# Kernel tuning notes

Hardware: AMD Instinct MI355X
Metric: run time of the kernel (lower is better)

Reference implementation:

```python
import jax, jax.numpy as jnp
import numpy as np
from jax import lax

N, C, F, W = 4096, 1, 15, 120
STRIDE = 10
NW = W // STRIDE            # 12 windows
P = F * (F - 1) // 2        # 105 pairs
HP = 2 * P + 4 * F          # 270 stacked stat rows
FC1_IN = 16 * HP * (NW - 2) # 43200
FC2, FC3, FCAST = 512, 128, 1
BN_EPS = 1e-5

# static pair indices, same order as generate(list(range(F)))
_II, _JJ = np.triu_indices(F, k=1)


def _fill(x):
    # numpy_fill: replace nan/inf with 0
    return jnp.where(jnp.isfinite(x), x, jnp.zeros_like(x))


def setup_inputs() -> dict:
    key = jax.random.key(0)
    ks = jax.random.split(key, 13)
    inp = {
        'data': jax.random.uniform(ks[0], (N, C, F, W), dtype=jnp.float32),
        'bn_gamma': jax.random.normal(ks[1], (C,), dtype=jnp.float32),
        'bn_beta': jax.random.normal(ks[2], (C,), dtype=jnp.float32),
        'bn_mean': jax.random.normal(ks[3], (C,), dtype=jnp.float32) * 0.1,
        'bn_var': jax.random.uniform(ks[4], (C,), dtype=jnp.float32) + 0.5,
        'conv_w': jax.random.normal(ks[5], (16, 1, 1, 3), dtype=jnp.float32) * 0.1,
        'conv_b': jax.random.normal(ks[6], (16,), dtype=jnp.float32) * 0.1,
        'fc1_w': jax.random.normal(ks[7], (FC2, FC1_IN), dtype=jnp.float32) * (1.0 / np.sqrt(FC1_IN)),
        'fc1_b': jax.random.normal(ks[8], (FC2,), dtype=jnp.float32) * 0.01,
        'fc2_w': jax.random.normal(ks[9], (FC3, FC2), dtype=jnp.float32) * (1.0 / np.sqrt(FC2)),
        'fc2_b': jax.random.normal(ks[10], (FC3,), dtype=jnp.float32) * 0.01,
        'fc3_w': jax.random.normal(ks[11], (FCAST, FC3), dtype=jnp.float32) * (1.0 / np.sqrt(FC3)),
        'fc3_b': jax.random.normal(ks[12], (FCAST,), dtype=jnp.float32) * 0.01,
    }
    return inp


def _features(data):
    # data: [N,C,F,W] -> windows [N,C,F,NW,S]
    S = STRIDE
    win = data.reshape(data.shape[0], data.shape[1], F, NW, S)
    mean = win.mean(axis=-1)                         # [N,C,F,NW]
    spread = win - mean[..., None]
    var_u = (spread * spread).sum(axis=-1) / (S - 1)  # unbiased, matches torch .std()
    std = jnp.sqrt(var_u)
    # pairwise cov / corr over (II, JJ)
    cov = (spread[:, :, _II] * spread[:, :, _JJ]).sum(axis=-1) / (S - 1)  # [N,C,P,NW]
    corr = _fill(cov / (std[:, :, _II] * std[:, :, _JJ]) * ((S - 1) / S))
    cov = _fill(cov)
    stdf = _fill(std)
    zs = _fill(mean / std)
    ret = _fill(win[..., -1] / win[..., 0] - 1.0)
    w = jnp.arange(1, S + 1, dtype=jnp.float32)
    w = w / w.sum()
    dl = _fill((win * w).sum(axis=-1))
    # concat along feature rows, order as in forward: corr,cov,std,zscore,return,decaylinear
    return jnp.concatenate([corr, cov, stdf, zs, ret, dl], axis=2)  # [N,C,HP,NW]


def reference(data, bn_gamma, bn_beta, bn_mean, bn_var, conv_w, conv_b,
              fc1_w, fc1_b, fc2_w, fc2_b, fc3_w, fc3_b):
    feat = _features(data)  # [N,1,HP,NW]
    # BatchNorm2d (eval mode, running stats)
    x = (feat - bn_mean[None, :, None, None]) * lax.rsqrt(bn_var + BN_EPS)[None, :, None, None]
    x = x * bn_gamma[None, :, None, None] + bn_beta[None, :, None, None]
    # Conv2d(1,16,(1,3)) valid padding
    x = lax.conv_general_dilated(x, conv_w, window_strides=(1, 1), padding='VALID',
                                 dimension_numbers=('NCHW', 'OIHW', 'NCHW'))
    x = jax.nn.relu(x + conv_b[None, :, None, None])  # [N,16,HP,NW-2]
    x = x.reshape(x.shape[0], -1)                      # [N, FC1_IN]
    # MLP head (dropout = identity in eval)
    x = jax.nn.relu(x @ fc1_w.T + fc1_b)
    x = jax.nn.sigmoid(x @ fc2_w.T + fc2_b)
    out = (x @ fc3_w.T + fc3_b)[:, 0]                  # fc3(...).T[0] -> [N]
    return out
```

## Files before the change

### kernel.cpp

```cpp
#include <hip/hip_runtime.h>
#include <cstdint>
#include <cstddef>


typedef _Float16 f16;
typedef f16 f16x2 __attribute__((ext_vector_type(2)));
typedef f16 f16x8 __attribute__((ext_vector_type(8)));
typedef float f32x4 __attribute__((ext_vector_type(4)));

#define CHUNK   2048
#define K_FC1   43200
#define KT_TOT  675
#define TILE_F  16384
#define HALF_F  8192

__device__ __forceinline__ float fillv(float x) { return isfinite(x) ? x : 0.0f; }

__global__ __launch_bounds__(256) void retile_w(const float* __restrict__ w,
                                                f16* __restrict__ Wt) {
    const int bid = blockIdx.x;
    const int nt = bid / KT_TOT, kt = bid % KT_TOT;
    const int t = threadIdx.x;
    f16* dst = Wt + (size_t)bid * TILE_F;
    #pragma unroll
    for (int j = 0; j < 8; ++j) {
        int q = t + 256 * j;
        int half = q >> 10, rr = (q >> 3) & 127, c = q & 7;
        const float* s = w + (size_t)(nt * 256 + half * 128 + rr) * K_FC1 + kt * 64 + c * 8;
        float4 x = *(const float4*)s;
        float4 y = *(const float4*)(s + 4);
        f16x8 o = { (f16)x.x, (f16)x.y, (f16)x.z, (f16)x.w,
                    (f16)y.x, (f16)y.y, (f16)y.z, (f16)y.w };
        int p = c ^ (rr & 7);
        *(f16x8*)(dst + (size_t)half * HALF_F + rr * 64 + p * 8) = o;
    }
}

__global__ __launch_bounds__(256) void stage_a(
    const float* __restrict__ data, const float* __restrict__ bn_g,
    const float* __restrict__ bn_b, const float* __restrict__ bn_m,
    const float* __restrict__ bn_v, const float* __restrict__ conv_w,
    const float* __restrict__ conv_b, f16* __restrict__ A16, int n0)
{
    __shared__ __align__(16) float pool[5400];
    __shared__ __align__(16) float feat[270 * 12];
    __shared__ float cwf[48];
    __shared__ float cbf[16];
    __shared__ int   pi[105], pj[105];

    float* raw = pool;
    f16*   cstage = (f16*)pool;

    const int t = threadIdx.x;
    const int n = n0 + blockIdx.x;
    const float4* src4 = (const float4*)(data + (size_t)n * 1800);
    for (int i = t; i < 450; i += 256) ((float4*)pool)[i] = src4[i];

    {
        float a  = bn_g[0] * rsqrtf(bn_v[0] + 1e-5f);
        float bb = bn_b[0] - bn_m[0] * a;
        if (t < 48) cwf[t] = conv_w[t] * a;
        if (t < 16) cbf[t] = conv_b[t] + bb * (conv_w[3 * t] + conv_w[3 * t + 1] + conv_w[3 * t + 2]);
    }
    if (t < 105) {
        int i = 0, rem = t;
        while (rem >= 14 - i) { rem -= 14 - i; ++i; }
        pi[t] = i; pj[t] = i + 1 + rem;
    }
    __syncthreads();

    if (t < 180) {
        int f = t / 12, w = t % 12;
        int base = f * 120 + w * 10;
        const float2* r2 = (const float2*)(raw + base);
        float2 p0 = r2[0], p1 = r2[1], p2 = r2[2], p3 = r2[3], p4 = r2[4];
        float x[10] = { p0.x, p0.y, p1.x, p1.y, p2.x, p2.y, p3.x, p3.y, p4.x, p4.y };
        float sum = 0.f;
        #pragma unroll
        for (int s = 0; s < 10; ++s) sum += x[s];
        float mean = sum * 0.1f;
        float ret = x[9] / x[0] - 1.0f;
        float dl = 0.f;
        #pragma unroll
        for (int s = 0; s < 10; ++s) dl += x[s] * ((float)(s + 1) * (1.0f / 55.0f));
        float var = 0.f;
        float d[10];
        #pragma unroll
        for (int s = 0; s < 10; ++s) { d[s] = x[s] - mean; var += d[s] * d[s]; }
        float2* w2p = (float2*)(raw + base);
        #pragma unroll
        for (int s = 0; s < 5; ++s) w2p[s] = make_float2(d[2 * s], d[2 * s + 1]);
        var *= (1.0f / 9.0f);
        float sd = sqrtf(var);
        feat[(210 + f) * 12 + w] = fillv(sd);
        feat[(225 + f) * 12 + w] = fillv(mean / sd);
        feat[(240 + f) * 12 + w] = fillv(ret);
        feat[(255 + f) * 12 + w] = fillv(dl);
    }
    __syncthreads();

    for (int q = t; q < 1260; q += 256) {
        int p = q / 12, w = q % 12;
        int i = pi[p], j = pj[p];
        const float2* ri = (const float2*)(raw + i * 120 + w * 10);
        const float2* rj = (const float2*)(raw + j * 120 + w * 10);
        float cv = 0.f;
        #pragma unroll
        for (int s = 0; s < 5; ++s) {
            float2 ai = ri[s], aj = rj[s];
            cv += ai.x * aj.x + ai.y * aj.y;
        }
        cv *= (1.0f / 9.0f);
        float si = feat[(210 + i) * 12 + w], sj = feat[(210 + j) * 12 + w];
        feat[p * 12 + w]         = fillv(cv / (si * sj) * 0.9f);
        feat[(105 + p) * 12 + w] = fillv(cv);
    }
    __syncthreads();

    const int s_idx = blockIdx.x;
    const int mt = s_idx >> 8, r256 = s_idx & 255;
    const int half = r256 >> 7, rloc = r256 & 127, rsw = r256 & 7;
    f16* abase = A16 + ((size_t)(mt * KT_TOT) * 2 + half) * HALF_F + (size_t)rloc * 64;

    for (int p = 0; p < 4; ++p) {
        #pragma unroll
        for (int j = 0; j < 5; ++j) {
            int item = t + (j << 8);
            if (item < 1080) {
                int h = item >> 2, ocl = item & 3, oc = (p << 2) + ocl;
                const float4* f4 = (const float4*)(feat + h * 12);
                float4 fa = f4[0], fb = f4[1], fc = f4[2];
                float fv[12] = { fa.x, fa.y, fa.z, fa.w,
                                 fb.x, fb.y, fb.z, fb.w,
                                 fc.x, fc.y, fc.z, fc.w };
                float w0 = cwf[oc * 3], w1 = cwf[oc * 3 + 1], w2 = cwf[oc * 3 + 2];
                float bz = cbf[oc];
                int kl = ocl * 2700 + h * 10;
                #pragma unroll
                for (int q = 0; q < 5; ++q) {
                    float y0 = fmaf(w2, fv[2 * q + 2], fmaf(w1, fv[2 * q + 1], fmaf(w0, fv[2 * q], bz)));
                    float y1 = fmaf(w2, fv[2 * q + 3], fmaf(w1, fv[2 * q + 2], fmaf(w0, fv[2 * q + 1], bz)));
                    y0 = fminf(fmaxf(y0, 0.f) * 0.00390625f, 65000.f);
                    y1 = fminf(fmaxf(y1, 0.f) * 0.00390625f, 65000.f);
                    *(f16x2*)(cstage + kl + 2 * q) = f16x2{ (f16)y0, (f16)y1 };
                }
            }
        }
        __syncthreads();
        #pragma unroll
        for (int j = 0; j < 6; ++j) {
            int u = t + (j << 8);
            if (u < 1350) {
                int U = p * 1350 + u;
                int kt = U >> 3, c = U & 7;
                f16x8 ov = *(const f16x8*)(cstage + u * 8);
                *(f16x8*)(abase + (size_t)kt * TILE_F + ((c ^ rsw) << 3)) = ov;
            }
        }
        __syncthreads();
    }
}

__global__ __launch_bounds__(512, 2) void gemm_fc1(const f16* __restrict__ A,
                                                   const f16* __restrict__ W,
                                                   float* __restrict__ Ysum)
{
    extern __shared__ f16 lds[];

    const int bid = blockIdx.x;
    const int mt = bid & 7;
    const int slot = bid >> 3;
    const int nt = slot & 1;
    const int sk = slot >> 1;
    const int kt0 = sk * 42 + (sk < 3 ? sk : 3);
    const int cnt = 42 + (sk < 3 ? 1 : 0);

    const int tid = threadIdx.x;
    const int wave = tid >> 6, lane = tid & 63;
    const int quad = lane >> 4, m16 = lane & 15;
    const int rsw = m16 & 7;
    const int wm = (wave & 1) << 6;
    const int wn = (wave >> 1) << 5;

    const f16* Ab = A + (size_t)(mt * KT_TOT + kt0) * TILE_F;
    const f16* Bb = W + (size_t)(nt * KT_TOT + kt0) * TILE_F;

    f32x4 acc[8][4] = {};
    f16x8 a[4][2], bA[2][2], bB[2][2];

#define STAGE_A(BUF, HALF, KI) do {                                            \
    const f16* g_ = Ab + (size_t)(KI) * TILE_F + (HALF) * HALF_F + tid * 8;    \
    f16* l_ = lds + (BUF) * TILE_F + (HALF) * HALF_F + tid * 8;                \
    __builtin_amdgcn_global_load_lds(                                          \
        (const __attribute__((address_space(1))) void*)g_,                     \
        (__attribute__((address_space(3))) void*)l_, 16, 0, 0);                \
    __builtin_amdgcn_global_load_lds(                                          \
        (const __attribute__((address_space(1))) void*)(g_ + 4096),            \
        (__attribute__((address_space(3))) void*)(l_ + 4096), 16, 0, 0);       \
} while (0)

#define STAGE_B(BUF, HALF, KI) do {                                            \
    const f16* g_ = Bb + (size_t)(KI) * TILE_F + (HALF) * HALF_F + tid * 8;    \
    f16* l_ = lds + 32768 + (BUF) * TILE_F + (HALF) * HALF_F + tid * 8;        \
    __builtin_amdgcn_global_load_lds(                                          \
        (const __attribute__((address_space(1))) void*)g_,                     \
        (__attribute__((address_space(3))) void*)l_, 16, 0, 0);                \
    __builtin_amdgcn_global_load_lds(                                          \
        (const __attribute__((address_space(1))) void*)(g_ + 4096),            \
        (__attribute__((address_space(3))) void*)(l_ + 4096), 16, 0, 0);       \
} while (0)

#define RD_A(MH, BUF) do {                                                     \
    _Pragma("unroll") for (int i2_ = 0; i2_ < 4; ++i2_)                        \
    _Pragma("unroll") for (int kh_ = 0; kh_ < 2; ++kh_)                        \
        a[i2_][kh_] = *(const f16x8*)(lds + (BUF) * TILE_F + (MH) * HALF_F     \
            + (wm + i2_ * 16 + m16) * 64 + (((kh_ * 4 + quad) ^ rsw) << 3));   \
} while (0)

#define RD_B(DST, NH, BUF) do {                                                \
    _Pragma("unroll") for (int j2_ = 0; j2_ < 2; ++j2_)                        \
    _Pragma("unroll") for (int kh_ = 0; kh_ < 2; ++kh_)                        \
        DST[j2_][kh_] = *(const f16x8*)(lds + 32768 + (BUF) * TILE_F           \
            + (NH) * HALF_F                                                    \
            + (wn + j2_ * 16 + m16) * 64 + (((kh_ * 4 + quad) ^ rsw) << 3));   \
} while (0)

#define MMA(IO, JO, BF) do {                                                   \
    _Pragma("unroll") for (int i2_ = 0; i2_ < 4; ++i2_)                        \
    _Pragma("unroll") for (int j2_ = 0; j2_ < 2; ++j2_)                        \
    _Pragma("unroll") for (int kh_ = 0; kh_ < 2; ++kh_)                        \
        acc[(IO) + i2_][(JO) + j2_] = __builtin_amdgcn_mfma_f32_16x16x32_f16(  \
            a[i2_][kh_], BF[j2_][kh_], acc[(IO) + i2_][(JO) + j2_], 0, 0, 0);  \
} while (0)

    STAGE_A(0, 0, 0);
    STAGE_B(0, 0, 0);
    STAGE_B(0, 1, 0);
    STAGE_A(0, 1, 0);
    asm volatile("s_waitcnt vmcnt(0)" ::: "memory");
    __builtin_amdgcn_s_barrier();

    #pragma unroll 1
    for (int ti = 0; ti < cnt; ++ti) {
        const int bc = ti & 1, bn = bc ^ 1;
        if (ti + 1 < cnt) {
            STAGE_A(bn, 0, ti + 1);
            STAGE_B(bn, 0, ti + 1);
            STAGE_B(bn, 1, ti + 1);
            STAGE_A(bn, 1, ti + 1);
        }
        RD_A(0, bc); RD_B(bA, 0, bc);
        __builtin_amdgcn_s_setprio(1);
        MMA(0, 0, bA);
        __builtin_amdgcn_s_setprio(0);
        RD_B(bB, 1, bc);
        __builtin_amdgcn_s_setprio(1);
        MMA(0, 2, bB);
        __builtin_amdgcn_s_setprio(0);
        RD_A(1, bc);
        __builtin_amdgcn_s_setprio(1);
        MMA(4, 2, bB);
        MMA(4, 0, bA);
        __builtin_amdgcn_s_setprio(0);
        if (ti + 1 < cnt) {
            asm volatile("s_waitcnt vmcnt(0)" ::: "memory");
            __builtin_amdgcn_s_barrier();
        }
    }

#undef STAGE_A
#undef STAGE_B
#undef RD_A
#undef RD_B
#undef MMA

    float* Yb = Ysum + (size_t)(mt * 256) * 512 + nt * 256;
    #pragma unroll
    for (int i = 0; i < 8; ++i) {
        const int row0 = (i >> 2) * 128 + wm + (i & 3) * 16 + quad * 4;
        #pragma unroll
        for (int j = 0; j < 4; ++j) {
            const int col = (j >> 1) * 128 + wn + (j & 1) * 16 + m16;
            #pragma unroll
            for (int r = 0; r < 4; ++r)
                unsafeAtomicAdd(&Yb[(size_t)(row0 + r) * 512 + col], acc[i][j][r]);
        }
    }
}

__global__ __launch_bounds__(128) void head_fc23(const float* __restrict__ y1s,
                                                 const float* __restrict__ b1,
                                                 const float* __restrict__ w2,
                                                 const float* __restrict__ b2,
                                                 const float* __restrict__ w3,
                                                 const float* __restrict__ b3,
                                                 float* __restrict__ out, int n0)
{
    __shared__ float Ys[8 * 512];
    __shared__ float Y2[8 * 128];
    const int t = threadIdx.x;
    const float4* yb = (const float4*)(y1s + (size_t)blockIdx.x * 8 * 512);
    const float4* b1v = (const float4*)b1;
    for (int i = t; i < 8 * 128; i += 128) {
        float4 s = yb[i];
        float4 bv = b1v[i & 127];
        float4 y;
        y.x = fmaxf(fmaf(s.x, 256.f, bv.x), 0.f);
        y.y = fmaxf(fmaf(s.y, 256.f, bv.y), 0.f);
        y.z = fmaxf(fmaf(s.z, 256.f, bv.z), 0.f);
        y.w = fmaxf(fmaf(s.w, 256.f, bv.w), 0.f);
        ((float4*)Ys)[i] = y;
    }
    __syncthreads();

    float acc[8];
    float bk = b2[t];
    #pragma unroll
    for (int s = 0; s < 8; ++s) acc[s] = bk;
    const float4* wr = (const float4*)(w2 + (size_t)t * 512);
    for (int jc = 0; jc < 128; ++jc) {
        float4 w4 = wr[jc];
        #pragma unroll
        for (int s = 0; s < 8; ++s) {
            float4 y4 = *(const float4*)(Ys + s * 512 + jc * 4);
            acc[s] += w4.x * y4.x + w4.y * y4.y + w4.z * y4.z + w4.w * y4.w;
        }
    }
    #pragma unroll
    for (int s = 0; s < 8; ++s) Y2[s * 128 + t] = 1.0f / (1.0f + expf(-acc[s]));
    __syncthreads();

    if (t < 8) {
        float sm = b3[0];
        #pragma unroll 4
        for (int k = 0; k < 128; ++k) sm += Y2[t * 128 + k] * w3[k];
        out[n0 + blockIdx.x * 8 + t] = sm;
    }
}

extern "C" void kernel_launch(void* const* d_in, const int* in_sizes, int n_in,
                              void* d_out, int out_size, void* d_ws, size_t ws_size,
                              hipStream_t stream)
{
    const float* data = (const float*)d_in[0];
    const float* bn_g = (const float*)d_in[1];
    const float* bn_b = (const float*)d_in[2];
    const float* bn_m = (const float*)d_in[3];
    const float* bn_v = (const float*)d_in[4];
    const float* cw   = (const float*)d_in[5];
    const float* cb   = (const float*)d_in[6];
    const float* fc1w = (const float*)d_in[7];
    const float* fc1b = (const float*)d_in[8];
    const float* fc2w = (const float*)d_in[9];
    const float* fc2b = (const float*)d_in[10];
    const float* fc3w = (const float*)d_in[11];
    const float* fc3b = (const float*)d_in[12];
    float* out = (float*)d_out;

    const size_t A16_BYTES = (size_t)CHUNK * K_FC1 * 2;
    const size_t W16_BYTES = (size_t)512 * K_FC1 * 2;
    const size_t Y1_BYTES  = (size_t)CHUNK * 512 * 4;
    if (ws_size < A16_BYTES + W16_BYTES + Y1_BYTES) return;

    char* ws = (char*)d_ws;
    f16*   A16 = (f16*)ws;
    f16*   W16 = (f16*)(ws + A16_BYTES);
    float* y1s = (float*)(ws + A16_BYTES + W16_BYTES);

    static int smem_set = 0;
    if (!smem_set) {
        hipFuncSetAttribute(reinterpret_cast<const void*>(gemm_fc1),
                            hipFuncAttributeMaxDynamicSharedMemorySize, 131072);
        smem_set = 1;
    }

    retile_w<<<2 * KT_TOT, 256, 0, stream>>>(fc1w, W16);

    for (int c = 0; c < 2; ++c) {
        int n0 = c * CHUNK;
        hipMemsetAsync(y1s, 0, Y1_BYTES, stream);
        stage_a<<<CHUNK, 256, 0, stream>>>(data, bn_g, bn_b, bn_m, bn_v, cw, cb, A16, n0);
        gemm_fc1<<<256, 512, 131072, stream>>>(A16, W16, y1s);
        head_fc23<<<CHUNK / 8, 128, 0, stream>>>(y1s, fc1b, fc2w, fc2b, fc3w, fc3b, out, n0);
    }
}
```

Before: 550.1 us.

## Restructure FC1 GEMM to 256x512 tiles with K=32 triple-buffered pipeline

The FC1 GEMM now uses 1024-thread blocks, each computing a full 256x512 output tile, in place of 256x256 tiles split across two N-halves. The K step drops from 64 to 32, staging is triple-buffered with two tiles in flight, and the split-K factor doubles to 32. The A and W retile layouts change to a 32-wide K tile with a rotate-style swizzle to match. The aim is to remove the duplicated A loads across N tiles and to hide load latency with deeper prefetch. In exchange, occupancy drops to one block per CU, the LDS footprint grows, and the number of atomic adds into the output doubles.

```diff
diff --git a/kernel.cpp b/kernel.cpp
--- a/kernel.cpp
+++ b/kernel.cpp
@@ -10,29 +10,29 @@
 
 #define CHUNK   2048
 #define K_FC1   43200
-#define KT_TOT  675
-#define TILE_F  16384
-#define HALF_F  8192
+#define KT32    1350
+#define TA_F    8192
+#define TB_F    16384
+#define BUF_F   24576
 
 __device__ __forceinline__ float fillv(float x) { return isfinite(x) ? x : 0.0f; }
 
 __global__ __launch_bounds__(256) void retile_w(const float* __restrict__ w,
                                                 f16* __restrict__ Wt) {
-    const int bid = blockIdx.x;
-    const int nt = bid / KT_TOT, kt = bid % KT_TOT;
+    const int kt = blockIdx.x;
     const int t = threadIdx.x;
-    f16* dst = Wt + (size_t)bid * TILE_F;
+    f16* dst = Wt + (size_t)kt * TB_F;
     #pragma unroll
     for (int j = 0; j < 8; ++j) {
         int q = t + 256 * j;
-        int half = q >> 10, rr = (q >> 3) & 127, c = q & 7;
-        const float* s = w + (size_t)(nt * 256 + half * 128 + rr) * K_FC1 + kt * 64 + c * 8;
+        int r = q >> 2, c = q & 3;
+        const float* s = w + (size_t)r * K_FC1 + kt * 32 + c * 8;
         float4 x = *(const float4*)s;
         float4 y = *(const float4*)(s + 4);
         f16x8 o = { (f16)x.x, (f16)x.y, (f16)x.z, (f16)x.w,
                     (f16)y.x, (f16)y.y, (f16)y.z, (f16)y.w };
-        int p = c ^ (rr & 7);
-        *(f16x8*)(dst + (size_t)half * HALF_F + rr * 64 + p * 8) = o;
+        int p = (c + (r >> 1)) & 3;
+        *(f16x8*)(dst + r * 32 + (p << 3)) = o;
     }
 }
 
@@ -119,8 +119,8 @@
 
     const int s_idx = blockIdx.x;
     const int mt = s_idx >> 8, r256 = s_idx & 255;
-    const int half = r256 >> 7, rloc = r256 & 127, rsw = r256 & 7;
-    f16* abase = A16 + ((size_t)(mt * KT_TOT) * 2 + half) * HALF_F + (size_t)rloc * 64;
+    const int srot = (r256 >> 1) & 3;
+    f16* abase = A16 + (size_t)mt * KT32 * TA_F + (size_t)r256 * 32;
 
     for (int p = 0; p < 4; ++p) {
         #pragma unroll
@@ -152,135 +152,107 @@
             int u = t + (j << 8);
             if (u < 1350) {
                 int U = p * 1350 + u;
-                int kt = U >> 3, c = U & 7;
+                int kt = U >> 2, c = U & 3;
                 f16x8 ov = *(const f16x8*)(cstage + u * 8);
-                *(f16x8*)(abase + (size_t)kt * TILE_F + ((c ^ rsw) << 3)) = ov;
+                *(f16x8*)(abase + (size_t)kt * TA_F + (((c + srot) & 3) << 3)) = ov;
             }
         }
         __syncthreads();
     }
 }
 
-__global__ __launch_bounds__(512, 2) void gemm_fc1(const f16* __restrict__ A,
-                                                   const f16* __restrict__ W,
-                                                   float* __restrict__ Ysum)
+__global__ __launch_bounds__(1024, 1) void gemm_fc1(const f16* __restrict__ A,
+                                                    const f16* __restrict__ W,
+                                                    float* __restrict__ Ysum)
 {
     extern __shared__ f16 lds[];
 
     const int bid = blockIdx.x;
-    const int mt = bid & 7;
-    const int slot = bid >> 3;
-    const int nt = slot & 1;
-    const int sk = slot >> 1;
-    const int kt0 = sk * 42 + (sk < 3 ? sk : 3);
-    const int cnt = 42 + (sk < 3 ? 1 : 0);
+    const int mt = (bid >> 3) & 7;
+    const int sk = (bid & 7) | (((bid >> 6) & 3) << 3);
+    const int kt0 = sk * 42 + (sk < 6 ? sk : 6);
+    const int cnt = 42 + (sk < 6 ? 1 : 0);
 
     const int tid = threadIdx.x;
     const int wave = tid >> 6, lane = tid & 63;
     const int quad = lane >> 4, m16 = lane & 15;
-    const int rsw = m16 & 7;
-    const int wm = (wave & 1) << 6;
-    const int wn = (wave >> 1) << 5;
-
-    const f16* Ab = A + (size_t)(mt * KT_TOT + kt0) * TILE_F;
-    const f16* Bb = W + (size_t)(nt * KT_TOT + kt0) * TILE_F;
-
-    f32x4 acc[8][4] = {};
-    f16x8 a[4][2], bA[2][2], bB[2][2];
-
-#define STAGE_A(BUF, HALF, KI) do {                                            \
-    const f16* g_ = Ab + (size_t)(KI) * TILE_F + (HALF) * HALF_F + tid * 8;    \
-    f16* l_ = lds + (BUF) * TILE_F + (HALF) * HALF_F + tid * 8;                \
+    const int srot = (quad + (m16 >> 1)) & 3;
+    const int wm = (wave & 3) << 6;
+    const int wn = (wave >> 2) << 7;
+
+    const f16* Ab = A + ((size_t)mt * KT32 + kt0) * TA_F;
+    const f16* Bb = W + (size_t)kt0 * TB_F;
+
+    f32x4 acc[4][8] = {};
+    f16x8 a[4], b[8];
+
+#define STAGE(BUF, KI) do {                                                    \
+    const f16* ga_ = Ab + (size_t)(KI) * TA_F + tid * 8;                       \
+    f16* la_ = lds + (BUF) * BUF_F + tid * 8;                                  \
     __builtin_amdgcn_global_load_lds(                                          \
-        (const __attribute__((address_space(1))) void*)g_,                     \
-        (__attribute__((address_space(3))) void*)l_, 16, 0, 0);                \
+        (const __attribute__((address_space(1))) void*)ga_,                    \
+        (__attribute__((address_space(3))) void*)la_, 16, 0, 0);               \
+    const f16* gb_ = Bb + (size_t)(KI) * TB_F + tid * 8;                       \
+    f16* lb_ = lds + (BUF) * BUF_F + TA_F + tid * 8;                           \
     __builtin_amdgcn_global_load_lds(                                          \
-        (const __attribute__((address_space(1))) void*)(g_ + 4096),            \
-        (__attribute__((address_space(3))) void*)(l_ + 4096), 16, 0, 0);       \
+        (const __attribute__((address_space(1))) void*)gb_,                    \
+        (__attribute__((address_space(3))) void*)lb_, 16, 0, 0);               \
+    __builtin_amdgcn_global_load_lds(                                          \
+        (const __attribute__((address_space(1))) void*)(gb_ + 8192),           \
+        (__attribute__((address_space(3))) void*)(lb_ + 8192), 16, 0, 0);      \
 } while (0)
 
-#define STAGE_B(BUF, HALF, KI) do {                                            \
-    const f16* g_ = Bb + (size_t)(KI) * TILE_F + (HALF) * HALF_F + tid * 8;    \
-    f16* l_ = lds + 32768 + (BUF) * TILE_F + (HALF) * HALF_F + tid * 8;        \
-    __builtin_amdgcn_global_load_lds(                                          \
-        (const __attribute__((address_space(1))) void*)g_,                     \
-        (__attribute__((address_space(3))) void*)l_, 16, 0, 0);                \
-    __builtin_amdgcn_global_load_lds(                                          \
-        (const __attribute__((address_space(1))) void*)(g_ + 4096),            \
-        (__attribute__((address_space(3))) void*)(l_ + 4096), 16, 0, 0);       \
+#define RD(BUF) do {                                                           \
+    const f16* Ax_ = lds + (BUF) * BUF_F;                                      \
+    const f16* Bx_ = lds + (BUF) * BUF_F + TA_F;                               \
+    _Pragma("unroll") for (int i2_ = 0; i2_ < 4; ++i2_)                        \
+        a[i2_] = *(const f16x8*)(Ax_ + (wm + i2_ * 16 + m16) * 32 + (srot << 3)); \
+    _Pragma("unroll") for (int j2_ = 0; j2_ < 8; ++j2_)                        \
+        b[j2_] = *(const f16x8*)(Bx_ + (wn + j2_ * 16 + m16) * 32 + (srot << 3)); \
 } while (0)
 
-#define RD_A(MH, BUF) do {                                                     \
+#define MMA() do {                                                             \
     _Pragma("unroll") for (int i2_ = 0; i2_ < 4; ++i2_)                        \
-    _Pragma("unroll") for (int kh_ = 0; kh_ < 2; ++kh_)                        \
-        a[i2_][kh_] = *(const f16x8*)(lds + (BUF) * TILE_F + (MH) * HALF_F     \
-            + (wm + i2_ * 16 + m16) * 64 + (((kh_ * 4 + quad) ^ rsw) << 3));   \
+    _Pragma("unroll") for (int j2_ = 0; j2_ < 8; ++j2_)                        \
+        acc[i2_][j2_] = __builtin_amdgcn_mfma_f32_16x16x32_f16(                \
+            a[i2_], b[j2_], acc[i2_][j2_], 0, 0, 0);                           \
 } while (0)
 
-#define RD_B(DST, NH, BUF) do {                                                \
-    _Pragma("unroll") for (int j2_ = 0; j2_ < 2; ++j2_)                        \
-    _Pragma("unroll") for (int kh_ = 0; kh_ < 2; ++kh_)                        \
-        DST[j2_][kh_] = *(const f16x8*)(lds + 32768 + (BUF) * TILE_F           \
-            + (NH) * HALF_F                                                    \
-            + (wn + j2_ * 16 + m16) * 64 + (((kh_ * 4 + quad) ^ rsw) << 3));   \
-} while (0)
-
-#define MMA(IO, JO, BF) do {                                                   \
-    _Pragma("unroll") for (int i2_ = 0; i2_ < 4; ++i2_)                        \
-    _Pragma("unroll") for (int j2_ = 0; j2_ < 2; ++j2_)                        \
-    _Pragma("unroll") for (int kh_ = 0; kh_ < 2; ++kh_)                        \
-        acc[(IO) + i2_][(JO) + j2_] = __builtin_amdgcn_mfma_f32_16x16x32_f16(  \
-            a[i2_][kh_], BF[j2_][kh_], acc[(IO) + i2_][(JO) + j2_], 0, 0, 0);  \
-} while (0)
-
-    STAGE_A(0, 0, 0);
-    STAGE_B(0, 0, 0);
-    STAGE_B(0, 1, 0);
-    STAGE_A(0, 1, 0);
-    asm volatile("s_waitcnt vmcnt(0)" ::: "memory");
+    STAGE(0, 0);
+    STAGE(1, 1);
+    asm volatile("s_waitcnt vmcnt(3)" ::: "memory");
     __builtin_amdgcn_s_barrier();
 
+    int cur = 0, nx2 = 2;
     #pragma unroll 1
     for (int ti = 0; ti < cnt; ++ti) {
-        const int bc = ti & 1, bn = bc ^ 1;
-        if (ti + 1 < cnt) {
-            STAGE_A(bn, 0, ti + 1);
-            STAGE_B(bn, 0, ti + 1);
-            STAGE_B(bn, 1, ti + 1);
-            STAGE_A(bn, 1, ti + 1);
-        }
-        RD_A(0, bc); RD_B(bA, 0, bc);
+        if (ti + 2 < cnt) STAGE(nx2, ti + 2);
+        RD(cur);
         __builtin_amdgcn_s_setprio(1);
-        MMA(0, 0, bA);
-        __builtin_amdgcn_s_setprio(0);
-        RD_B(bB, 1, bc);
-        __builtin_amdgcn_s_setprio(1);
-        MMA(0, 2, bB);
-        __builtin_amdgcn_s_setprio(0);
-        RD_A(1, bc);
-        __builtin_amdgcn_s_setprio(1);
-        MMA(4, 2, bB);
-        MMA(4, 0, bA);
+        MMA();
         __builtin_amdgcn_s_setprio(0);
         if (ti + 1 < cnt) {
-            asm volatile("s_waitcnt vmcnt(0)" ::: "memory");
+            if (ti + 2 < cnt)
+                asm volatile("s_waitcnt vmcnt(3)" ::: "memory");
+            else
+                asm volatile("s_waitcnt vmcnt(0)" ::: "memory");
             __builtin_amdgcn_s_barrier();
         }
-    }
-
-#undef STAGE_A
-#undef STAGE_B
-#undef RD_A
-#undef RD_B
+        cur = (cur == 2) ? 0 : cur + 1;
+        nx2 = (nx2 == 2) ? 0 : nx2 + 1;
+    }
+
+#undef STAGE
+#undef RD
 #undef MMA
 
-    float* Yb = Ysum + (size_t)(mt * 256) * 512 + nt * 256;
+    float* Yb = Ysum + (size_t)(mt * 256) * 512;
     #pragma unroll
-    for (int i = 0; i < 8; ++i) {
-        const int row0 = (i >> 2) * 128 + wm + (i & 3) * 16 + quad * 4;
-        #pragma unroll
-        for (int j = 0; j < 4; ++j) {
-            const int col = (j >> 1) * 128 + wn + (j & 1) * 16 + m16;
+    for (int i = 0; i < 4; ++i) {
+        const int row0 = wm + i * 16 + quad * 4;
+        #pragma unroll
+        for (int j = 0; j < 8; ++j) {
+            const int col = wn + j * 16 + m16;
             #pragma unroll
             for (int r = 0; r < 4; ++r)
                 unsafeAtomicAdd(&Yb[(size_t)(row0 + r) * 512 + col], acc[i][j][r]);
@@ -370,17 +342,17 @@
     static int smem_set = 0;
     if (!smem_set) {
         hipFuncSetAttribute(reinterpret_cast<const void*>(gemm_fc1),
-                            hipFuncAttributeMaxDynamicSharedMemorySize, 131072);
+                            hipFuncAttributeMaxDynamicSharedMemorySize, 147456);
         smem_set = 1;
     }
 
-    retile_w<<<2 * KT_TOT, 256, 0, stream>>>(fc1w, W16);
+    retile_w<<<KT32, 256, 0, stream>>>(fc1w, W16);
 
     for (int c = 0; c < 2; ++c) {
         int n0 = c * CHUNK;
         hipMemsetAsync(y1s, 0, Y1_BYTES, stream);
         stage_a<<<CHUNK, 256, 0, stream>>>(data, bn_g, bn_b, bn_m, bn_v, cw, cb, A16, n0);
-        gemm_fc1<<<256, 512, 131072, stream>>>(A16, W16, y1s);
+        gemm_fc1<<<256, 1024, 147456, stream>>>(A16, W16, y1s);
         head_fc23<<<CHUNK / 8, 128, 0, stream>>>(y1s, fc1b, fc2w, fc2b, fc3w, fc3b, out, n0);
     }
 }
```

Result: slower. 2.070 ms (+276.3%).

## Fuse conv+ReLU A-operand generation into FC1 GEMM prologue from compact features

Applied to the files above, without the earlier changes.

Instead of materialising the full 43200-wide fp16 conv output per sample in global memory, a new kernel writes only the 3240 batch-normalised features per sample. The GEMM then computes the conv, ReLU and fp16 conversion on the fly while loading each A tile into LDS. The A operand no longer makes a round trip through HBM, which is 16x larger than the features. The cost is conv arithmetic, integer division and redundant feature loads inside the GEMM's pipelined loop, plus serial CONV work after the waitcnt that may stall the MMAs.

```diff
diff --git a/kernel.cpp b/kernel.cpp
--- a/kernel.cpp
+++ b/kernel.cpp
@@ -9,10 +9,12 @@
 typedef float f32x4 __attribute__((ext_vector_type(4)));
 
 #define CHUNK   2048
+#define NTOT    4096
 #define K_FC1   43200
 #define KT_TOT  675
 #define TILE_F  16384
 #define HALF_F  8192
+#define FPS     3240
 
 __device__ __forceinline__ float fillv(float x) { return isfinite(x) ? x : 0.0f; }
 
@@ -36,32 +38,19 @@
     }
 }
 
-__global__ __launch_bounds__(256) void stage_a(
+__global__ __launch_bounds__(256) void feat_k(
     const float* __restrict__ data, const float* __restrict__ bn_g,
     const float* __restrict__ bn_b, const float* __restrict__ bn_m,
-    const float* __restrict__ bn_v, const float* __restrict__ conv_w,
-    const float* __restrict__ conv_b, f16* __restrict__ A16, int n0)
+    const float* __restrict__ bn_v, float* __restrict__ FEAT)
 {
-    __shared__ __align__(16) float pool[5400];
-    __shared__ __align__(16) float feat[270 * 12];
-    __shared__ float cwf[48];
-    __shared__ float cbf[16];
+    __shared__ __align__(16) float raw[1800];
+    __shared__ __align__(16) float feat[FPS];
     __shared__ int   pi[105], pj[105];
 
-    float* raw = pool;
-    f16*   cstage = (f16*)pool;
-
     const int t = threadIdx.x;
-    const int n = n0 + blockIdx.x;
+    const int n = blockIdx.x;
     const float4* src4 = (const float4*)(data + (size_t)n * 1800);
-    for (int i = t; i < 450; i += 256) ((float4*)pool)[i] = src4[i];
-
-    {
-        float a  = bn_g[0] * rsqrtf(bn_v[0] + 1e-5f);
-        float bb = bn_b[0] - bn_m[0] * a;
-        if (t < 48) cwf[t] = conv_w[t] * a;
-        if (t < 16) cbf[t] = conv_b[t] + bb * (conv_w[3 * t] + conv_w[3 * t + 1] + conv_w[3 * t + 2]);
-    }
+    for (int i = t; i < 450; i += 256) ((float4*)raw)[i] = src4[i];
     if (t < 105) {
         int i = 0, rem = t;
         while (rem >= 14 - i) { rem -= 14 - i; ++i; }
@@ -117,53 +106,21 @@
     }
     __syncthreads();
 
-    const int s_idx = blockIdx.x;
-    const int mt = s_idx >> 8, r256 = s_idx & 255;
-    const int half = r256 >> 7, rloc = r256 & 127, rsw = r256 & 7;
-    f16* abase = A16 + ((size_t)(mt * KT_TOT) * 2 + half) * HALF_F + (size_t)rloc * 64;
-
-    for (int p = 0; p < 4; ++p) {
-        #pragma unroll
-        for (int j = 0; j < 5; ++j) {
-            int item = t + (j << 8);
-            if (item < 1080) {
-                int h = item >> 2, ocl = item & 3, oc = (p << 2) + ocl;
-                const float4* f4 = (const float4*)(feat + h * 12);
-                float4 fa = f4[0], fb = f4[1], fc = f4[2];
-                float fv[12] = { fa.x, fa.y, fa.z, fa.w,
-                                 fb.x, fb.y, fb.z, fb.w,
-                                 fc.x, fc.y, fc.z, fc.w };
-                float w0 = cwf[oc * 3], w1 = cwf[oc * 3 + 1], w2 = cwf[oc * 3 + 2];
-                float bz = cbf[oc];
-                int kl = ocl * 2700 + h * 10;
-                #pragma unroll
-                for (int q = 0; q < 5; ++q) {
-                    float y0 = fmaf(w2, fv[2 * q + 2], fmaf(w1, fv[2 * q + 1], fmaf(w0, fv[2 * q], bz)));
-                    float y1 = fmaf(w2, fv[2 * q + 3], fmaf(w1, fv[2 * q + 2], fmaf(w0, fv[2 * q + 1], bz)));
-                    y0 = fminf(fmaxf(y0, 0.f) * 0.00390625f, 65000.f);
-                    y1 = fminf(fmaxf(y1, 0.f) * 0.00390625f, 65000.f);
-                    *(f16x2*)(cstage + kl + 2 * q) = f16x2{ (f16)y0, (f16)y1 };
-                }
-            }
-        }
-        __syncthreads();
-        #pragma unroll
-        for (int j = 0; j < 6; ++j) {
-            int u = t + (j << 8);
-            if (u < 1350) {
-                int U = p * 1350 + u;
-                int kt = U >> 3, c = U & 7;
-                f16x8 ov = *(const f16x8*)(cstage + u * 8);
-                *(f16x8*)(abase + (size_t)kt * TILE_F + ((c ^ rsw) << 3)) = ov;
-            }
-        }
-        __syncthreads();
-    }
-}
-
-__global__ __launch_bounds__(512, 2) void gemm_fc1(const f16* __restrict__ A,
-                                                   const f16* __restrict__ W,
-                                                   float* __restrict__ Ysum)
+    float a  = bn_g[0] * rsqrtf(bn_v[0] + 1e-5f);
+    float bb = bn_b[0] - bn_m[0] * a;
+    float4* dst = (float4*)(FEAT + (size_t)n * FPS);
+    for (int i = t; i < FPS / 4; i += 256) {
+        float4 v = ((const float4*)feat)[i];
+        v.x = fmaf(v.x, a, bb); v.y = fmaf(v.y, a, bb);
+        v.z = fmaf(v.z, a, bb); v.w = fmaf(v.w, a, bb);
+        dst[i] = v;
+    }
+}
+
+__global__ __launch_bounds__(512, 2) void gemm_fused(
+    const float* __restrict__ FEAT, const f16* __restrict__ W,
+    const float* __restrict__ cw, const float* __restrict__ cb,
+    float* __restrict__ Ysum, int n0)
 {
     extern __shared__ f16 lds[];
 
@@ -182,33 +139,74 @@
     const int wm = (wave & 1) << 6;
     const int wn = (wave >> 1) << 5;
 
-    const f16* Ab = A + (size_t)(mt * KT_TOT + kt0) * TILE_F;
+    const int cr = tid & 255, dp = tid >> 8;
+    const int crsw = cr & 7;
+    const float* featN = FEAT + (size_t)(n0 + mt * 256 + cr) * FPS;
+
     const f16* Bb = W + (size_t)(nt * KT_TOT + kt0) * TILE_F;
 
     f32x4 acc[8][4] = {};
     f16x8 a[4][2], bA[2][2], bB[2][2];
-
-#define STAGE_A(BUF, HALF, KI) do {                                            \
-    const f16* g_ = Ab + (size_t)(KI) * TILE_F + (HALF) * HALF_F + tid * 8;    \
-    f16* l_ = lds + (BUF) * TILE_F + (HALF) * HALF_F + tid * 8;                \
+    float4 fq0, fq1, fq2, fq3, fq4, fq5, fq6, fq7, fq8, fq9, fq10, fq11;
+
+#define STAGE_B(BUF, KI) do {                                                  \
+    const f16* g_ = Bb + (size_t)(KI) * TILE_F + tid * 8;                      \
+    f16* l_ = lds + 32768 + (BUF) * TILE_F + tid * 8;                          \
     __builtin_amdgcn_global_load_lds(                                          \
         (const __attribute__((address_space(1))) void*)g_,                     \
         (__attribute__((address_space(3))) void*)l_, 16, 0, 0);                \
     __builtin_amdgcn_global_load_lds(                                          \
         (const __attribute__((address_space(1))) void*)(g_ + 4096),            \
         (__attribute__((address_space(3))) void*)(l_ + 4096), 16, 0, 0);       \
+    __builtin_amdgcn_global_load_lds(                                          \
+        (const __attribute__((address_space(1))) void*)(g_ + 8192),            \
+        (__attribute__((address_space(3))) void*)(l_ + 8192), 16, 0, 0);       \
+    __builtin_amdgcn_global_load_lds(                                          \
+        (const __attribute__((address_space(1))) void*)(g_ + 12288),           \
+        (__attribute__((address_space(3))) void*)(l_ + 12288), 16, 0, 0);      \
 } while (0)
 
-#define STAGE_B(BUF, HALF, KI) do {                                            \
-    const f16* g_ = Bb + (size_t)(KI) * TILE_F + (HALF) * HALF_F + tid * 8;    \
-    f16* l_ = lds + 32768 + (BUF) * TILE_F + (HALF) * HALF_F + tid * 8;        \
-    __builtin_amdgcn_global_load_lds(                                          \
-        (const __attribute__((address_space(1))) void*)g_,                     \
-        (__attribute__((address_space(3))) void*)l_, 16, 0, 0);                \
-    __builtin_amdgcn_global_load_lds(                                          \
-        (const __attribute__((address_space(1))) void*)(g_ + 4096),            \
-        (__attribute__((address_space(3))) void*)(l_ + 4096), 16, 0, 0);       \
-} while (0)
+#define FQ(DI) fq##DI
+#define FLOAD1(DI, A_, B_, C_) do {                                            \
+    int kb_ = (kt0 + (KI_)) * 64;                                              \
+    int d0_ = kb_ / 10, nd_ = (kb_ + 63) / 10 - d0_ + 1;                       \
+    if (dp + 2 * (DI) < nd_) {                                                 \
+        int dd_ = d0_ + dp + 2 * (DI);                                         \
+        int oc_ = dd_ / 270, hh_ = dd_ - oc_ * 270;                            \
+        const float4* fp_ = (const float4*)(featN + hh_ * 12);                 \
+        A_ = fp_[0]; B_ = fp_[1]; C_ = fp_[2];                                 \
+    } } while (0)
+#define FLOAD(KI) do { const int KI_ = (KI);                                   \
+    FLOAD1(0, fq0, fq1, fq2);  FLOAD1(1, fq3, fq4, fq5);                       \
+    FLOAD1(2, fq6, fq7, fq8);  FLOAD1(3, fq9, fq10, fq11); } while (0)
+
+#define CONV1(DI, A_, B_, C_) do {                                             \
+    int kb_ = (kt0 + (KI_)) * 64;                                              \
+    int d0_ = kb_ / 10, nd_ = (kb_ + 63) / 10 - d0_ + 1;                       \
+    if (dp + 2 * (DI) < nd_) {                                                 \
+        int dd_ = d0_ + dp + 2 * (DI);                                         \
+        int oc_ = dd_ / 270;                                                   \
+        float w0_ = cw[oc_ * 3], w1_ = cw[oc_ * 3 + 1], w2_ = cw[oc_ * 3 + 2]; \
+        float bz_ = cb[oc_];                                                   \
+        float fv_[12] = { A_.x, A_.y, A_.z, A_.w, B_.x, B_.y, B_.z, B_.w,      \
+                          C_.x, C_.y, C_.z, C_.w };                            \
+        int cb0_ = dd_ * 10 - kb_;                                             \
+        _Pragma("unroll") for (int wp_ = 0; wp_ < 5; ++wp_) {                  \
+            int c_ = cb0_ + 2 * wp_;                                           \
+            if (c_ >= 0 && c_ <= 62) {                                         \
+                float y0_ = fmaf(w2_, fv_[2*wp_+2], fmaf(w1_, fv_[2*wp_+1],    \
+                                 fmaf(w0_, fv_[2*wp_], bz_)));                 \
+                float y1_ = fmaf(w2_, fv_[2*wp_+3], fmaf(w1_, fv_[2*wp_+2],    \
+                                 fmaf(w0_, fv_[2*wp_+1], bz_)));               \
+                y0_ = fminf(fmaxf(y0_, 0.f) * 0.00390625f, 65000.f);           \
+                y1_ = fminf(fmaxf(y1_, 0.f) * 0.00390625f, 65000.f);           \
+                *(f16x2*)(ab_ + (((c_ >> 3) ^ crsw) << 3) + (c_ & 7)) =        \
+                    f16x2{ (f16)y0_, (f16)y1_ };                               \
+            } } } } while (0)
+#define CONV(BUF, KI) do { const int KI_ = (KI);                               \
+    f16* ab_ = lds + (BUF) * TILE_F + (cr >> 7) * HALF_F + (size_t)(cr & 127) * 64; \
+    CONV1(0, fq0, fq1, fq2);  CONV1(1, fq3, fq4, fq5);                         \
+    CONV1(2, fq6, fq7, fq8);  CONV1(3, fq9, fq10, fq11); } while (0)
 
 #define RD_A(MH, BUF) do {                                                     \
     _Pragma("unroll") for (int i2_ = 0; i2_ < 4; ++i2_)                        \
@@ -233,21 +231,19 @@
             a[i2_][kh_], BF[j2_][kh_], acc[(IO) + i2_][(JO) + j2_], 0, 0, 0);  \
 } while (0)
 
-    STAGE_A(0, 0, 0);
-    STAGE_B(0, 0, 0);
-    STAGE_B(0, 1, 0);
-    STAGE_A(0, 1, 0);
+    STAGE_B(0, 0);
+    FLOAD(0);
     asm volatile("s_waitcnt vmcnt(0)" ::: "memory");
+    CONV(0, 0);
+    asm volatile("s_waitcnt lgkmcnt(0)" ::: "memory");
     __builtin_amdgcn_s_barrier();
 
     #pragma unroll 1
     for (int ti = 0; ti < cnt; ++ti) {
         const int bc = ti & 1, bn = bc ^ 1;
         if (ti + 1 < cnt) {
-            STAGE_A(bn, 0, ti + 1);
-            STAGE_B(bn, 0, ti + 1);
-            STAGE_B(bn, 1, ti + 1);
-            STAGE_A(bn, 1, ti + 1);
+            STAGE_B(bn, ti + 1);
+            FLOAD(ti + 1);
         }
         RD_A(0, bc); RD_B(bA, 0, bc);
         __builtin_amdgcn_s_setprio(1);
@@ -264,12 +260,18 @@
         __builtin_amdgcn_s_setprio(0);
         if (ti + 1 < cnt) {
             asm volatile("s_waitcnt vmcnt(0)" ::: "memory");
+            CONV(bn, ti + 1);
+            asm volatile("s_waitcnt lgkmcnt(0)" ::: "memory");
             __builtin_amdgcn_s_barrier();
         }
     }
 
-#undef STAGE_A
 #undef STAGE_B
+#undef FLOAD
+#undef FLOAD1
+#undef CONV
+#undef CONV1
+#undef FQ
 #undef RD_A
 #undef RD_B
 #undef MMA
@@ -357,30 +359,30 @@
     const float* fc3b = (const float*)d_in[12];
     float* out = (float*)d_out;
 
-    const size_t A16_BYTES = (size_t)CHUNK * K_FC1 * 2;
-    const size_t W16_BYTES = (size_t)512 * K_FC1 * 2;
-    const size_t Y1_BYTES  = (size_t)CHUNK * 512 * 4;
-    if (ws_size < A16_BYTES + W16_BYTES + Y1_BYTES) return;
+    const size_t FEAT_BYTES = (size_t)NTOT * FPS * 4;
+    const size_t W16_BYTES  = (size_t)512 * K_FC1 * 2;
+    const size_t Y1_BYTES   = (size_t)CHUNK * 512 * 4;
+    if (ws_size < FEAT_BYTES + W16_BYTES + Y1_BYTES) return;
 
     char* ws = (char*)d_ws;
-    f16*   A16 = (f16*)ws;
-    f16*   W16 = (f16*)(ws + A16_BYTES);
-    float* y1s = (float*)(ws + A16_BYTES + W16_BYTES);
+    float* FEAT = (float*)ws;
+    f16*   W16  = (f16*)(ws + FEAT_BYTES);
+    float* y1s  = (float*)(ws + FEAT_BYTES + W16_BYTES);
 
     static int smem_set = 0;
     if (!smem_set) {
-        hipFuncSetAttribute(reinterpret_cast<const void*>(gemm_fc1),
+        hipFuncSetAttribute(reinterpret_cast<const void*>(gemm_fused),
                             hipFuncAttributeMaxDynamicSharedMemorySize, 131072);
         smem_set = 1;
     }
 
     retile_w<<<2 * KT_TOT, 256, 0, stream>>>(fc1w, W16);
+    feat_k<<<NTOT, 256, 0, stream>>>(data, bn_g, bn_b, bn_m, bn_v, FEAT);
 
     for (int c = 0; c < 2; ++c) {
         int n0 = c * CHUNK;
         hipMemsetAsync(y1s, 0, Y1_BYTES, stream);
-        stage_a<<<CHUNK, 256, 0, stream>>>(data, bn_g, bn_b, bn_m, bn_v, cw, cb, A16, n0);
-        gemm_fc1<<<256, 512, 131072, stream>>>(A16, W16, y1s);
+        gemm_fused<<<256, 512, 131072, stream>>>(FEAT, W16, cw, cb, y1s, n0);
         head_fc23<<<CHUNK / 8, 128, 0, stream>>>(y1s, fc1b, fc2w, fc2b, fc3w, fc3b, out, n0);
     }
 }
```

After: 775.7 us. 41.0% more time.
